# Kernel tuning notes

Measured on AMD Instinct MI355X. Metric: run time of the kernel, lower is better.

Reference implementation:

```python
import jax, jax.numpy as jnp
import numpy as np

NUM_HEAD = 8
DIM_MODEL = 512
DIM_HEAD = DIM_MODEL // NUM_HEAD
LN_EPS = 1e-5


def setup_inputs() -> dict:
    key = jax.random.key(0)
    ks = jax.random.split(key, 12)
    B, L, D = 4, 2048, DIM_MODEL
    s = 0.02
    return {
        "x": jax.random.normal(ks[0], (B, L, D), dtype=jnp.float32),
        "Wq": jax.random.normal(ks[1], (D, D), dtype=jnp.float32) * s,
        "bq": jnp.zeros((D,), dtype=jnp.float32),
        "Wk": jax.random.normal(ks[2], (D, D), dtype=jnp.float32) * s,
        "bk": jnp.zeros((D,), dtype=jnp.float32),
        "Wv": jax.random.normal(ks[3], (D, D), dtype=jnp.float32) * s,
        "bv": jnp.zeros((D,), dtype=jnp.float32),
        "Wo": jax.random.normal(ks[4], (D, D), dtype=jnp.float32) * s,
        "bo": jnp.zeros((D,), dtype=jnp.float32),
        "gamma": jnp.ones((D,), dtype=jnp.float32),
        "beta": jnp.zeros((D,), dtype=jnp.float32),
    }


def reference(x, Wq, bq, Wk, bk, Wv, bv, Wo, bo, gamma, beta):
    B, L, D = x.shape
    H, dh = NUM_HEAD, D // NUM_HEAD
    # QKV projections (torch Linear: x @ W.T + b)
    Q = x @ Wq.T + bq
    K = x @ Wk.T + bk
    V = x @ Wv.T + bv
    # Faithful to the torch code: contiguous view(B*H, L, dh)
    Q = Q.reshape(B * H, L, dh)
    K = K.reshape(B * H, L, dh)
    V = V.reshape(B * H, L, dh)
    scale = dh ** (-0.5)
    # [B*H, L, L] scores, scaled, softmax over keys
    attn = jax.nn.softmax(jnp.einsum("bqd,bkd->bqk", Q, K) * scale, axis=-1)
    context = jnp.einsum("bqk,bkd->bqd", attn, V)  # [B*H, L, dh]
    context = context.reshape(B, L, D)
    out = context @ Wo.T + bo
    out = out + x  # residual (dropout p=0.0 -> identity)
    # LayerNorm over last dim
    mu = jnp.mean(out, axis=-1, keepdims=True)
    var = jnp.mean(jnp.square(out - mu), axis=-1, keepdims=True)
    out = (out - mu) / jnp.sqrt(var + LN_EPS) * gamma + beta
    return out
```

## Files before the change

### kernel.cpp

```cpp
#include <hip/hip_runtime.h>

typedef __bf16 bf16;
typedef __bf16 bf16x4 __attribute__((ext_vector_type(4)));
typedef __bf16 bf16x8 __attribute__((ext_vector_type(8)));
typedef float f32x4 __attribute__((ext_vector_type(4)));

#define MFMA16(A, B, C) __builtin_amdgcn_mfma_f32_16x16x32_bf16((A), (B), (C), 0, 0, 0)

constexpr int Dm   = 512;
constexpr int Lm   = 2048;
constexpr int DH   = 64;
constexpr int Mrows = 8192;
constexpr int NHEADS = 32;

__device__ __forceinline__ void gload16(const void* g, void* l) {
    __builtin_amdgcn_global_load_lds(
        (const __attribute__((address_space(1))) void*)g,
        (__attribute__((address_space(3))) void*)l, 16, 0, 0);
}

__global__ __launch_bounds__(256)
void cvt_kernel(const float* __restrict__ x, const float* __restrict__ Wq,
                const float* __restrict__ Wk, const float* __restrict__ Wv,
                const float* __restrict__ Wo,
                bf16* __restrict__ xb, bf16* __restrict__ Wqb, bf16* __restrict__ Wkb,
                bf16* __restrict__ Wvb, bf16* __restrict__ Wob)
{
    size_t i = ((size_t)blockIdx.x * 256 + threadIdx.x) * 4;
    const float* src; bf16* dst; size_t off;
    if (i < (size_t)Mrows * Dm) {
        src = x; dst = xb; off = i;
    } else {
        size_t r = i - (size_t)Mrows * Dm;
        int w = (int)(r >> 18);
        off = r & 262143;
        src = (w == 0) ? Wq : (w == 1) ? Wk : (w == 2) ? Wv : Wo;
        dst = (w == 0) ? Wqb : (w == 1) ? Wkb : (w == 2) ? Wvb : Wob;
    }
    float4 v = *reinterpret_cast<const float4*>(src + off);
    bf16x4 o; o[0] = (bf16)v.x; o[1] = (bf16)v.y; o[2] = (bf16)v.z; o[3] = (bf16)v.w;
    *reinterpret_cast<bf16x4*>(dst + off) = o;
}

__global__ __launch_bounds__(256)
void qkv_gemm(const bf16* __restrict__ xb,
              const bf16* __restrict__ Wqb, const float* __restrict__ bq,
              const bf16* __restrict__ Wkb, const float* __restrict__ bk,
              const bf16* __restrict__ Wvb, const float* __restrict__ bv,
              bf16* __restrict__ Qo, bf16* __restrict__ Ko, bf16* __restrict__ Vo)
{
    __shared__ bf16 Asm[128 * 64];
    __shared__ bf16 Bsm[128 * 64];

    const int z = blockIdx.z;
    const bf16* W = (z == 0) ? Wqb : (z == 1) ? Wkb : Wvb;
    const float* bias = (z == 0) ? bq : (z == 1) ? bk : bv;
    bf16* out = (z == 0) ? Qo : (z == 1) ? Ko : Vo;

    const int tid = threadIdx.x;
    const int row0 = blockIdx.y * 128;
    const int col0 = blockIdx.x * 128;

    const int wv = tid >> 6;
    const int ln = tid & 63;
    const int wr = wv >> 1, wc = wv & 1;
    const int lr = ln & 15;
    const int lg = ln >> 4;

    const int srow_b = wv * 8 + (ln >> 3);
    const int ssc = ((ln & 7) ^ (ln >> 3)) * 8;

    f32x4 acc[4][4] = {};

    for (int kt = 0; kt < Dm; kt += 64) {
        __syncthreads();
        #pragma unroll
        for (int j = 0; j < 4; ++j) {
            const int row = j * 32 + srow_b;
            const int base = (j * 256 + wv * 64) * 8;
            gload16(xb + (size_t)(row0 + row) * Dm + kt + ssc, &Asm[base]);
            gload16(W + (size_t)(col0 + row) * Dm + kt + ssc, &Bsm[base]);
        }
        __syncthreads();

        #pragma unroll
        for (int ks = 0; ks < 2; ++ks) {
            bf16x8 af[4], bfv[4];
            #pragma unroll
            for (int m = 0; m < 4; ++m) {
                const int R = wr * 64 + m * 16 + lr;
                af[m] = *reinterpret_cast<const bf16x8*>(&Asm[R * 64 + (((ks * 4 + lg) ^ (R & 7)) * 8)]);
            }
            #pragma unroll
            for (int n = 0; n < 4; ++n) {
                const int R = wc * 64 + n * 16 + lr;
                bfv[n] = *reinterpret_cast<const bf16x8*>(&Bsm[R * 64 + (((ks * 4 + lg) ^ (R & 7)) * 8)]);
            }
            #pragma unroll
            for (int m = 0; m < 4; ++m)
                #pragma unroll
                for (int n = 0; n < 4; ++n)
                    acc[m][n] = MFMA16(af[m], bfv[n], acc[m][n]);
        }
    }

    #pragma unroll
    for (int m = 0; m < 4; ++m)
        #pragma unroll
        for (int n = 0; n < 4; ++n)
            #pragma unroll
            for (int i = 0; i < 4; ++i) {
                int r = row0 + wr * 64 + m * 16 + lg * 4 + i;
                int c = col0 + wc * 64 + n * 16 + lr;
                out[(size_t)r * Dm + c] = (bf16)(acc[m][n][i] + bias[c]);
            }
}

__global__ __launch_bounds__(256)
void oproj_gemm(const bf16* __restrict__ ctx, const bf16* __restrict__ Wob,
                const float* __restrict__ bo, const float* __restrict__ x,
                float* __restrict__ tmp)
{
    __shared__ bf16 Asm[128 * 64];
    __shared__ bf16 Bsm[128 * 64];

    const int tid = threadIdx.x;
    const int row0 = blockIdx.y * 128;
    const int col0 = blockIdx.x * 128;

    const int wv = tid >> 6;
    const int ln = tid & 63;
    const int wr = wv >> 1, wc = wv & 1;
    const int lr = ln & 15;
    const int lg = ln >> 4;

    const int srow_b = wv * 8 + (ln >> 3);
    const int ssc = ((ln & 7) ^ (ln >> 3)) * 8;

    f32x4 acc[4][4] = {};

    for (int kt = 0; kt < Dm; kt += 64) {
        __syncthreads();
        #pragma unroll
        for (int j = 0; j < 4; ++j) {
            const int row = j * 32 + srow_b;
            const int base = (j * 256 + wv * 64) * 8;
            gload16(ctx + (size_t)(row0 + row) * Dm + kt + ssc, &Asm[base]);
            gload16(Wob + (size_t)(col0 + row) * Dm + kt + ssc, &Bsm[base]);
        }
        __syncthreads();

        #pragma unroll
        for (int ks = 0; ks < 2; ++ks) {
            bf16x8 af[4], bfv[4];
            #pragma unroll
            for (int m = 0; m < 4; ++m) {
                const int R = wr * 64 + m * 16 + lr;
                af[m] = *reinterpret_cast<const bf16x8*>(&Asm[R * 64 + (((ks * 4 + lg) ^ (R & 7)) * 8)]);
            }
            #pragma unroll
            for (int n = 0; n < 4; ++n) {
                const int R = wc * 64 + n * 16 + lr;
                bfv[n] = *reinterpret_cast<const bf16x8*>(&Bsm[R * 64 + (((ks * 4 + lg) ^ (R & 7)) * 8)]);
            }
            #pragma unroll
            for (int m = 0; m < 4; ++m)
                #pragma unroll
                for (int n = 0; n < 4; ++n)
                    acc[m][n] = MFMA16(af[m], bfv[n], acc[m][n]);
        }
    }

    #pragma unroll
    for (int m = 0; m < 4; ++m)
        #pragma unroll
        for (int n = 0; n < 4; ++n)
            #pragma unroll
            for (int i = 0; i < 4; ++i) {
                int r = row0 + wr * 64 + m * 16 + lg * 4 + i;
                int c = col0 + wc * 64 + n * 16 + lr;
                tmp[(size_t)r * Dm + c] = acc[m][n][i] + bo[c] + x[(size_t)r * Dm + c];
            }
}

__global__ __launch_bounds__(256)
void vt_kernel(const bf16* __restrict__ V, bf16* __restrict__ Vt)
{
    __shared__ bf16 T[64 * 72];
    const int head = blockIdx.y;
    const int k0 = blockIdx.x * 64;
    const size_t hb = (size_t)head * (Lm * DH);
    const int tid = threadIdx.x;
    const int r = tid >> 2;
    const int seg = (tid & 3) * 16;

    {
        const bf16* src = &V[hb + (size_t)(k0 + r) * DH + seg];
        *reinterpret_cast<bf16x8*>(&T[r * 72 + seg])     = reinterpret_cast<const bf16x8*>(src)[0];
        *reinterpret_cast<bf16x8*>(&T[r * 72 + seg + 8]) = reinterpret_cast<const bf16x8*>(src)[1];
    }
    __syncthreads();
    bf16 o[16];
    #pragma unroll
    for (int j = 0; j < 16; ++j) o[j] = T[(seg + j) * 72 + r];
    *reinterpret_cast<bf16x8*>(&Vt[hb + (size_t)r * Lm + k0 + seg])     = *reinterpret_cast<bf16x8*>(&o[0]);
    *reinterpret_cast<bf16x8*>(&Vt[hb + (size_t)r * Lm + k0 + seg + 8]) = *reinterpret_cast<bf16x8*>(&o[8]);
}

__global__ __launch_bounds__(512)
void flash_attn(const bf16* __restrict__ Q, const bf16* __restrict__ K,
                const bf16* __restrict__ Vt, bf16* __restrict__ ctx)
{
    __shared__ bf16 Ksm[64 * 72];
    __shared__ bf16 Vsm[64 * 72];
    __shared__ bf16 Psm[128 * 72];

    const int head = blockIdx.y;
    const int q0 = blockIdx.x * 128;
    const size_t hb = (size_t)head * (Lm * DH);

    const int tid = threadIdx.x;
    const int wv = tid >> 6;
    const int ln = tid & 63;
    const int lr = ln & 15;
    const int lg = ln >> 4;

    const int srow = tid >> 3;
    const int sseg = (tid & 7) * 8;

    const float qscale = 0.125f * 1.44269504088896340736f;
    bf16x8 qf[2];
    {
        const int qrow = q0 + wv * 16 + lr;
        #pragma unroll
        for (int s = 0; s < 2; ++s) {
            bf16x8 t = *reinterpret_cast<const bf16x8*>(&Q[hb + (size_t)qrow * DH + s * 32 + lg * 8]);
            #pragma unroll
            for (int j = 0; j < 8; ++j) qf[s][j] = (bf16)((float)t[j] * qscale);
        }
    }

    f32x4 cfr[4] = {};
    float lsum[4] = {};

    bf16x8 kreg = *reinterpret_cast<const bf16x8*>(&K[hb + (size_t)srow * DH + sseg]);
    bf16x8 vreg = *reinterpret_cast<const bf16x8*>(&Vt[hb + (size_t)srow * Lm + sseg]);

    constexpr int NT = Lm / 64;
    for (int t = 0; t < NT; ++t) {
        __syncthreads();
        *reinterpret_cast<bf16x8*>(&Ksm[srow * 72 + sseg]) = kreg;
        *reinterpret_cast<bf16x8*>(&Vsm[srow * 72 + sseg]) = vreg;
        if (t + 1 < NT) {
            const int kn = (t + 1) * 64;
            kreg = *reinterpret_cast<const bf16x8*>(&K[hb + (size_t)(kn + srow) * DH + sseg]);
            vreg = *reinterpret_cast<const bf16x8*>(&Vt[hb + (size_t)srow * Lm + kn + sseg]);
        }
        __syncthreads();

        f32x4 sfr[4] = {};
        __builtin_amdgcn_s_setprio(1);
        #pragma unroll
        for (int s = 0; s < 2; ++s)
            #pragma unroll
            for (int g = 0; g < 4; ++g) {
                bf16x8 kf = *reinterpret_cast<const bf16x8*>(&Ksm[(g * 16 + lr) * 72 + s * 32 + lg * 8]);
                sfr[g] = MFMA16(qf[s], kf, sfr[g]);
            }
        __builtin_amdgcn_s_setprio(0);

        #pragma unroll
        for (int g = 0; g < 4; ++g)
            #pragma unroll
            for (int i = 0; i < 4; ++i) {
                float p = exp2f(sfr[g][i]);
                lsum[i] += p;
                Psm[(wv * 16 + lg * 4 + i) * 72 + g * 16 + lr] = (bf16)p;
            }

        __builtin_amdgcn_s_setprio(1);
        #pragma unroll
        for (int s = 0; s < 2; ++s) {
            bf16x8 pa = *reinterpret_cast<const bf16x8*>(&Psm[(wv * 16 + lr) * 72 + s * 32 + lg * 8]);
            #pragma unroll
            for (int n = 0; n < 4; ++n) {
                bf16x8 vb = *reinterpret_cast<const bf16x8*>(&Vsm[(n * 16 + lr) * 72 + s * 32 + lg * 8]);
                cfr[n] = MFMA16(pa, vb, cfr[n]);
            }
        }
        __builtin_amdgcn_s_setprio(0);
    }

    #pragma unroll
    for (int off = 1; off < 16; off <<= 1)
        #pragma unroll
        for (int i = 0; i < 4; ++i) lsum[i] += __shfl_xor(lsum[i], off);

    float inv[4];
    #pragma unroll
    for (int i = 0; i < 4; ++i) inv[i] = 1.f / lsum[i];
    #pragma unroll
    for (int n = 0; n < 4; ++n)
        #pragma unroll
        for (int i = 0; i < 4; ++i) {
            int q = q0 + wv * 16 + lg * 4 + i;
            int d = n * 16 + lr;
            ctx[hb + (size_t)q * DH + d] = (bf16)(cfr[n][i] * inv[i]);
        }
}

__global__ __launch_bounds__(128)
void ln_kernel(const float* __restrict__ tmp, const float* __restrict__ gamma,
               const float* __restrict__ beta, float* __restrict__ out)
{
    const int row = blockIdx.x;
    const int tid = threadIdx.x;
    const int wv = tid >> 6;
    const int ln = tid & 63;

    float4 v = reinterpret_cast<const float4*>(tmp + (size_t)row * Dm)[tid];
    float s = v.x + v.y + v.z + v.w;
    float sq = v.x * v.x + v.y * v.y + v.z * v.z + v.w * v.w;

    #pragma unroll
    for (int off = 32; off > 0; off >>= 1) {
        s += __shfl_down(s, off);
        sq += __shfl_down(sq, off);
    }
    __shared__ float red[4];
    if (ln == 0) { red[wv * 2] = s; red[wv * 2 + 1] = sq; }
    __syncthreads();
    s = red[0] + red[2];
    sq = red[1] + red[3];

    const float mu = s * (1.f / Dm);
    const float var = sq * (1.f / Dm) - mu * mu;
    const float rstd = rsqrtf(var + 1e-5f);

    float4 g = reinterpret_cast<const float4*>(gamma)[tid];
    float4 b = reinterpret_cast<const float4*>(beta)[tid];
    float4 o;
    o.x = (v.x - mu) * rstd * g.x + b.x;
    o.y = (v.y - mu) * rstd * g.y + b.y;
    o.z = (v.z - mu) * rstd * g.z + b.z;
    o.w = (v.w - mu) * rstd * g.w + b.w;
    reinterpret_cast<float4*>(out + (size_t)row * Dm)[tid] = o;
}

extern "C" void kernel_launch(void* const* d_in, const int* in_sizes, int n_in,
                              void* d_out, int out_size, void* d_ws, size_t ws_size,
                              hipStream_t stream)
{
    const float* x  = (const float*)d_in[0];
    const float* Wq = (const float*)d_in[1];
    const float* bq = (const float*)d_in[2];
    const float* Wk = (const float*)d_in[3];
    const float* bk = (const float*)d_in[4];
    const float* Wv = (const float*)d_in[5];
    const float* bv = (const float*)d_in[6];
    const float* Wo = (const float*)d_in[7];
    const float* bo = (const float*)d_in[8];
    const float* gamma = (const float*)d_in[9];
    const float* beta  = (const float*)d_in[10];
    float* out = (float*)d_out;

    const size_t MD = (size_t)Mrows * Dm;
    const size_t WD = (size_t)Dm * Dm;
    char* p = (char*)d_ws;
    bf16* xb  = (bf16*)p;                 p += MD * 2;
    bf16* Qw  = (bf16*)p;                 p += MD * 2;
    bf16* Kw  = (bf16*)p;                 p += MD * 2;
    bf16* Vw  = (bf16*)p;                 p += MD * 2;
    bf16* Vtw = (bf16*)p;                 p += MD * 2;
    bf16* Wqb = (bf16*)p;                 p += WD * 2;
    bf16* Wkb = (bf16*)p;                 p += WD * 2;
    bf16* Wvb = (bf16*)p;                 p += WD * 2;
    bf16* Wob = (bf16*)p;                 p += WD * 2;
    float* Tw = (float*)d_ws;
    bf16* Cw = Vw;

    {
        const size_t total = MD + 4 * WD;
        cvt_kernel<<<dim3((unsigned)(total / (256 * 4))), 256, 0, stream>>>(
            x, Wq, Wk, Wv, Wo, xb, Wqb, Wkb, Wvb, Wob);
    }

    qkv_gemm<<<dim3(Dm / 128, Mrows / 128, 3), 256, 0, stream>>>(
        xb, Wqb, bq, Wkb, bk, Wvb, bv, Qw, Kw, Vw);

    vt_kernel<<<dim3(Lm / 64, NHEADS), 256, 0, stream>>>(Vw, Vtw);

    flash_attn<<<dim3(Lm / 128, NHEADS), 512, 0, stream>>>(Qw, Kw, Vtw, Cw);

    oproj_gemm<<<dim3(Dm / 128, Mrows / 128), 256, 0, stream>>>(Cw, Wob, bo, x, Tw);

    ln_kernel<<<dim3(Mrows), 128, 0, stream>>>(Tw, gamma, beta, out);
}
```

Baseline: 204.2 us.

## Double-buffer K/V tiles in LDS and pad shared rows to 76

K and V tiles are now double-buffered in shared memory. The next tile's register-staged data is written into the alternate buffer while the current tile is consumed, which cuts the two barriers per iteration down to one at the end of the loop. The shared row stride also changes from 72 to 76 elements, presumably to alter the LDS bank mapping. The trade-offs are doubled K/V shared-memory use, which may lower occupancy, and a 152-byte row stride that is no longer 16-byte aligned for the 128-bit LDS vector loads.

```diff
diff --git a/kernel.cpp b/kernel.cpp
--- a/kernel.cpp
+++ b/kernel.cpp
@@ -211,9 +211,9 @@
 void flash_attn(const bf16* __restrict__ Q, const bf16* __restrict__ K,
                 const bf16* __restrict__ Vt, bf16* __restrict__ ctx)
 {
-    __shared__ bf16 Ksm[64 * 72];
-    __shared__ bf16 Vsm[64 * 72];
-    __shared__ bf16 Psm[128 * 72];
+    __shared__ bf16 Ksm[2][64 * 76];
+    __shared__ bf16 Vsm[2][64 * 76];
+    __shared__ bf16 Psm[128 * 76];
 
     const int head = blockIdx.y;
     const int q0 = blockIdx.x * 128;
@@ -227,6 +227,7 @@
 
     const int srow = tid >> 3;
     const int sseg = (tid & 7) * 8;
+    const int sb = srow * 76 + sseg;
 
     const float qscale = 0.125f * 1.44269504088896340736f;
     bf16x8 qf[2];
@@ -243,20 +244,28 @@
     f32x4 cfr[4] = {};
     float lsum[4] = {};
 
-    bf16x8 kreg = *reinterpret_cast<const bf16x8*>(&K[hb + (size_t)srow * DH + sseg]);
-    bf16x8 vreg = *reinterpret_cast<const bf16x8*>(&Vt[hb + (size_t)srow * Lm + sseg]);
+    const bf16* Kp = &K[hb + (size_t)srow * DH + sseg];
+    const bf16* Vp = &Vt[hb + (size_t)srow * Lm + sseg];
+
+    bf16x8 kreg = *reinterpret_cast<const bf16x8*>(Kp);
+    bf16x8 vreg = *reinterpret_cast<const bf16x8*>(Vp);
+    *reinterpret_cast<bf16x8*>(&Ksm[0][sb]) = kreg;
+    *reinterpret_cast<bf16x8*>(&Vsm[0][sb]) = vreg;
+    kreg = *reinterpret_cast<const bf16x8*>(Kp + 64 * DH);
+    vreg = *reinterpret_cast<const bf16x8*>(Vp + 64);
+    __syncthreads();
 
     constexpr int NT = Lm / 64;
     for (int t = 0; t < NT; ++t) {
-        __syncthreads();
-        *reinterpret_cast<bf16x8*>(&Ksm[srow * 72 + sseg]) = kreg;
-        *reinterpret_cast<bf16x8*>(&Vsm[srow * 72 + sseg]) = vreg;
+        const int cur = t & 1;
         if (t + 1 < NT) {
-            const int kn = (t + 1) * 64;
-            kreg = *reinterpret_cast<const bf16x8*>(&K[hb + (size_t)(kn + srow) * DH + sseg]);
-            vreg = *reinterpret_cast<const bf16x8*>(&Vt[hb + (size_t)srow * Lm + kn + sseg]);
-        }
-        __syncthreads();
+            *reinterpret_cast<bf16x8*>(&Ksm[cur ^ 1][sb]) = kreg;
+            *reinterpret_cast<bf16x8*>(&Vsm[cur ^ 1][sb]) = vreg;
+        }
+        if (t + 2 < NT) {
+            kreg = *reinterpret_cast<const bf16x8*>(Kp + (size_t)(t + 2) * 64 * DH);
+            vreg = *reinterpret_cast<const bf16x8*>(Vp + (t + 2) * 64);
+        }
 
         f32x4 sfr[4] = {};
         __builtin_amdgcn_s_setprio(1);
@@ -264,7 +273,7 @@
         for (int s = 0; s < 2; ++s)
             #pragma unroll
             for (int g = 0; g < 4; ++g) {
-                bf16x8 kf = *reinterpret_cast<const bf16x8*>(&Ksm[(g * 16 + lr) * 72 + s * 32 + lg * 8]);
+                bf16x8 kf = *reinterpret_cast<const bf16x8*>(&Ksm[cur][(g * 16 + lr) * 76 + s * 32 + lg * 8]);
                 sfr[g] = MFMA16(qf[s], kf, sfr[g]);
             }
         __builtin_amdgcn_s_setprio(0);
@@ -275,20 +284,22 @@
             for (int i = 0; i < 4; ++i) {
                 float p = exp2f(sfr[g][i]);
                 lsum[i] += p;
-                Psm[(wv * 16 + lg * 4 + i) * 72 + g * 16 + lr] = (bf16)p;
+                Psm[(wv * 16 + lg * 4 + i) * 76 + g * 16 + lr] = (bf16)p;
             }
 
         __builtin_amdgcn_s_setprio(1);
         #pragma unroll
         for (int s = 0; s < 2; ++s) {
-            bf16x8 pa = *reinterpret_cast<const bf16x8*>(&Psm[(wv * 16 + lr) * 72 + s * 32 + lg * 8]);
+            bf16x8 pa = *reinterpret_cast<const bf16x8*>(&Psm[(wv * 16 + lr) * 76 + s * 32 + lg * 8]);
             #pragma unroll
             for (int n = 0; n < 4; ++n) {
-                bf16x8 vb = *reinterpret_cast<const bf16x8*>(&Vsm[(n * 16 + lr) * 72 + s * 32 + lg * 8]);
+                bf16x8 vb = *reinterpret_cast<const bf16x8*>(&Vsm[cur][(n * 16 + lr) * 76 + s * 32 + lg * 8]);
                 cfr[n] = MFMA16(pa, vb, cfr[n]);
             }
         }
         __builtin_amdgcn_s_setprio(0);
+
+        __syncthreads();
     }
 
     #pragma unroll
```

After: 203.7 us. No clear change (-0.2%).
